# Performance work log

Hardware: AMD Instinct MI355X
Metric: run time of the kernel (lower is better)

The kernel has to match this reference:

```python
import jax, jax.numpy as jnp
import numpy as np

B, T, LEADS = 16, 3600, 12
P = 9; S = T // P          # 400 patches
DP = 128                   # d_patch / codebook dim
DM = 256                   # d_model
H = 8; HD = DM // H        # heads, head_dim
NL = 6                     # transformer layers
V = 512                    # codebook size
RH = 64                    # residual CNN hidden
BETA = 0.25


def conv1d(x, w, b, pad, stride=1):
    # x: (B,C,T), w: (O,I,K) pytorch layout
    y = jax.lax.conv_general_dilated(x, w, (stride,), [(pad, pad)],
                                     dimension_numbers=('NCH', 'OIH', 'NCH'))
    return y + b[None, :, None]


def layer_norm(x, g, b, eps=1e-5):
    m = jnp.mean(x, -1, keepdims=True)
    v = jnp.mean(jnp.square(x - m), -1, keepdims=True)
    return (x - m) * jax.lax.rsqrt(v + eps) * g + b


def gelu(x):
    return jax.nn.gelu(x, approximate=False)  # matches torch nn.GELU default


def setup_inputs() -> dict:
    key = jax.random.key(0)
    ks = iter(jax.random.split(key, 64))
    def rn(shape, s=0.02):
        return (s * jax.random.normal(next(ks), shape)).astype(jnp.float32)
    inp = {}
    inp['x'] = jax.random.normal(next(ks), (B, T, LEADS), dtype=jnp.float32)
    # PatchEncoder
    inp['pe_w1'] = rn((DP // 2, LEADS, 3)); inp['pe_b1'] = rn((DP // 2,))
    inp['pe_w2'] = rn((DP, DP // 2, 3));    inp['pe_b2'] = rn((DP,))
    inp['pe_pw'] = rn((DP, DP, P));         inp['pe_pb'] = rn((DP,))
    inp['pe_g'] = jnp.ones((DP,), jnp.float32); inp['pe_bb'] = jnp.zeros((DP,), jnp.float32)
    # VQ codebook (uniform +-1/V as in torch init)
    inp['cb'] = jax.random.uniform(next(ks), (V, DP), jnp.float32, -1.0 / V, 1.0 / V)
    # token_proj
    inp['tp_w'] = rn((DM, DP)); inp['tp_b'] = rn((DM,))
    inp['tp_g'] = jnp.ones((DM,), jnp.float32); inp['tp_bb'] = jnp.zeros((DM,), jnp.float32)
    # transformer layers (stacked over NL)
    inp['ln1_g'] = jnp.ones((NL, DM), jnp.float32); inp['ln1_b'] = jnp.zeros((NL, DM), jnp.float32)
    inp['inw'] = rn((NL, 3 * DM, DM));  inp['inb'] = rn((NL, 3 * DM))
    inp['ow'] = rn((NL, DM, DM));       inp['ob'] = rn((NL, DM))
    inp['ln2_g'] = jnp.ones((NL, DM), jnp.float32); inp['ln2_b'] = jnp.zeros((NL, DM), jnp.float32)
    inp['f1w'] = rn((NL, 4 * DM, DM));  inp['f1b'] = rn((NL, 4 * DM))
    inp['f2w'] = rn((NL, DM, 4 * DM));  inp['f2b'] = rn((NL, DM))
    inp['slopes'] = (1.0 + 0.1 * jax.random.normal(next(ks), (NL, H))).astype(jnp.float32)
    # final norm
    inp['fn_g'] = jnp.ones((DM,), jnp.float32); inp['fn_b'] = jnp.zeros((DM,), jnp.float32)
    # PatchDecoder: ConvTranspose1d weight (in=DM, out=DM//2, k=P)
    inp['up_w'] = rn((DM, DM // 2, P)); inp['up_b'] = rn((DM // 2,))
    inp['d1w'] = rn((DM // 4, DM // 2, 5)); inp['d1b'] = rn((DM // 4,))
    inp['d2w'] = rn((LEADS, DM // 4, 3));   inp['d2b'] = rn((LEADS,))
    # ResidualCNN
    inp['r1w'] = rn((RH, LEADS, 7)); inp['r1b'] = rn((RH,))
    inp['r2w'] = rn((RH, RH, 5));    inp['r2b'] = rn((RH,))
    inp['r3w'] = rn((RH, RH, 3));    inp['r3b'] = rn((RH,))
    inp['r4w'] = rn((LEADS, RH, 1)); inp['r4b'] = rn((LEADS,))
    inp['alpha'] = jnp.float32(0.5)
    return inp


def _forward(x, pe_w1, pe_b1, pe_w2, pe_b2, pe_pw, pe_pb, pe_g, pe_bb, cb,
             tp_w, tp_b, tp_g, tp_bb, ln1_g, ln1_b, inw, inb, ow, ob,
             ln2_g, ln2_b, f1w, f1b, f2w, f2b, slopes, fn_g, fn_b,
             up_w, up_b, d1w, d1b, d2w, d2b,
             r1w, r1b, r2w, r2b, r3w, r3b, r4w, r4b, alpha):
    Bs = x.shape[0]
    sg = jax.lax.stop_gradient
    # --- PatchEncoder: (B,T,L) -> (B,S,DP) ---
    h = x.transpose(0, 2, 1)                      # (B,L,T)
    h = gelu(conv1d(h, pe_w1, pe_b1, 1))
    h = gelu(conv1d(h, pe_w2, pe_b2, 1))
    h = conv1d(h, pe_pw, pe_pb, 0, stride=P)      # (B,DP,S)
    z_e = layer_norm(h.transpose(0, 2, 1), pe_g, pe_bb)   # (B,S,DP)
    # --- VQ codebook with STE ---
    zf = z_e.reshape(-1, DP)
    dist = (jnp.sum(zf * zf, 1, keepdims=True) + jnp.sum(cb * cb, 1)[None, :]
            - 2.0 * zf @ cb.T)                    # (B*S, V)
    tokens = jnp.argmin(dist, axis=1)
    zq = cb[tokens]                               # (B*S, DP)
    commit = jnp.mean(jnp.square(sg(zq) - zf)) + BETA * jnp.mean(jnp.square(zq - sg(zf)))
    zq_ste = (zf + sg(zq - zf)).reshape(Bs, S, DP)
    # --- token projection ---
    h = layer_norm(zq_ste @ tp_w.T + tp_b, tp_g, tp_bb)   # (B,S,DM)
    # --- transformer with relative-position bias ---
    pos = jnp.arange(S)
    rel = jnp.abs(pos[:, None] - pos[None, :]).astype(h.dtype)  # (S,S)
    scale = 1.0 / jnp.sqrt(jnp.float32(HD))
    for l in range(NL):
        bias = -jnp.abs(slopes[l])[:, None, None] * rel[None]   # (H,S,S)
        xn = layer_norm(h, ln1_g[l], ln1_b[l])
        qkv = xn @ inw[l].T + inb[l]
        q, k, v = jnp.split(qkv, 3, axis=-1)
        q = q.reshape(Bs, S, H, HD); k = k.reshape(Bs, S, H, HD); v = v.reshape(Bs, S, H, HD)
        logits = jnp.einsum('bqhd,bkhd->bhqk', q, k) * scale + bias[None]
        attn = jax.nn.softmax(logits, axis=-1)
        o = jnp.einsum('bhqk,bkhd->bqhd', attn, v).reshape(Bs, S, DM)
        h = h + o @ ow[l].T + ob[l]
        hn = layer_norm(h, ln2_g[l], ln2_b[l])
        h = h + gelu(hn @ f1w[l].T + f1b[l]) @ f2w[l].T + f2b[l]
    h = layer_norm(h, fn_g, fn_b)
    # --- PatchDecoder: (B,S,DM) -> (B,T,L) ---
    hc = h.transpose(0, 2, 1)                     # (B,DM,S)
    # ConvTranspose1d with stride==kernel==P, no overlap -> pure einsum
    u = jnp.einsum('bds,dok->bosk', hc, up_w).reshape(Bs, DM // 2, S * P) + up_b[None, :, None]
    u = gelu(u)
    u = gelu(conv1d(u, d1w, d1b, 2))
    u = conv1d(u, d2w, d2b, 1)                    # (B,L,T)
    decoded = u.transpose(0, 2, 1)
    # --- ResidualCNN on raw input ---
    r = x.transpose(0, 2, 1)
    r = gelu(conv1d(r, r1w, r1b, 3))
    r = gelu(conv1d(r, r2w, r2b, 2))
    r = gelu(conv1d(r, r3w, r3b, 1))
    r = conv1d(r, r4w, r4b, 0)
    residual = r.transpose(0, 2, 1)
    out = decoded + alpha * residual
    return out, commit


def reference(x, pe_w1, pe_b1, pe_w2, pe_b2, pe_pw, pe_pb, pe_g, pe_bb, cb,
              tp_w, tp_b, tp_g, tp_bb, ln1_g, ln1_b, inw, inb, ow, ob,
              ln2_g, ln2_b, f1w, f1b, f2w, f2b, slopes, fn_g, fn_b,
              up_w, up_b, d1w, d1b, d2w, d2b,
              r1w, r1b, r2w, r2b, r3w, r3b, r4w, r4b, alpha):
    return _forward(x, pe_w1, pe_b1, pe_w2, pe_b2, pe_pw, pe_pb, pe_g, pe_bb, cb,
                    tp_w, tp_b, tp_g, tp_bb, ln1_g, ln1_b, inw, inb, ow, ob,
                    ln2_g, ln2_b, f1w, f1b, f2w, f2b, slopes, fn_g, fn_b,
                    up_w, up_b, d1w, d1b, d2w, d2b,
                    r1w, r1b, r2w, r2b, r3w, r3b, r4w, r4b, alpha)
```

## Files before the change

kernel.cpp:

```cpp
#include <hip/hip_runtime.h>
#include <hip/hip_bf16.h>
#include <math.h>

#define BATCH 16
#define TLEN 3600
#define LEADS 12
#define PP 9
#define SS 400
#define DP 128
#define DM 256
#define NH 8
#define HD 32
#define NLAY 6
#define VV 512
#define RH 64

typedef __attribute__((ext_vector_type(8))) short short8b;
typedef __attribute__((ext_vector_type(4))) float f32x4;

__device__ __forceinline__ float gelu_f(float x) {
    return 0.5f * x * (1.0f + erff(x * 0.70710678118654752f));
}

__device__ __forceinline__ unsigned short f2bf(float f) {
// ... 151 lines not shown
                l8[e] = (short)f2bf(vv[e] - bf2f(h));
            }
        }
        *(short8b*)&Ah[row][q * 8] = h8;
        *(short8b*)&Al[row][q * 8] = l8;
    }
    f32x4 acc[2][8];
    #pragma unroll
    for (int i = 0; i < 2; ++i)
        #pragma unroll
        for (int j = 0; j < 8; ++j) acc[i][j] = (f32x4){0.f, 0.f, 0.f, 0.f};
    for (int k = 0; k < 3; ++k) {
        __syncthreads();
        for (int u = tid; u < 128 * 8; u += 256) {
            int co = u >> 3, q = u & 7;
            *(short8b*)&Wh_s[co][q * 8] = *(const short8b*)&wh[((size_t)(k * 128 + co)) * 64 + q * 8];
            *(short8b*)&Wl_s[co][q * 8] = *(const short8b*)&wl[((size_t)(k * 128 + co)) * 64 + q * 8];
        }
        __syncthreads();
        #pragma unroll
        for (int c32 = 0; c32 < 2; ++c32) {
            short8b ah0 = *(const short8b*)&Ah[w * 32 + fr + k][c32 * 32 + kg];
            short8b ah1 = *(const short8b*)&Ah[w * 32 + 16 + fr + k][c32 * 32 + kg];
            short8b al0 = *(const short8b*)&Al[w * 32 + fr + k][c32 * 32 + kg];
            short8b al1 = *(const short8b*)&Al[w * 32 + 16 + fr + k][c32 * 32 + kg];
            #pragma unroll
            for (int j = 0; j < 8; ++j) {
                short8b bh = *(const short8b*)&Wh_s[j * 16 + fr][c32 * 32 + kg];
                short8b bl = *(const short8b*)&Wl_s[j * 16 + fr][c32 * 32 + kg];
                acc[0][j] = __builtin_amdgcn_mfma_f32_16x16x32_bf16(ah0, bh, acc[0][j], 0, 0, 0);
                acc[0][j] = __builtin_amdgcn_mfma_f32_16x16x32_bf16(ah0, bl, acc[0][j], 0, 0, 0);
                acc[0][j] = __builtin_amdgcn_mfma_f32_16x16x32_bf16(al0, bh, acc[0][j], 0, 0, 0);
                acc[1][j] = __builtin_amdgcn_mfma_f32_16x16x32_bf16(ah1, bh, acc[1][j], 0, 0, 0);
                acc[1][j] = __builtin_amdgcn_mfma_f32_16x16x32_bf16(ah1, bl, acc[1][j], 0, 0, 0);
                acc[1][j] = __builtin_amdgcn_mfma_f32_16x16x32_bf16(al1, bh, acc[1][j], 0, 0, 0);
            }
        }
    }
    const int orow = (lane >> 4) * 4, ocol = lane & 15;
    #pragma unroll
    for (int i = 0; i < 2; ++i)
        #pragma unroll
        for (int j = 0; j < 8; ++j) {
            const int co = j * 16 + ocol;
            const float bv = bias[co];
            #pragma unroll
            for (int r = 0; r < 4; ++r) {
                int t = t0 + w * 32 + i * 16 + orow + r;
                if (t < TLEN) {
                    int s = t / PP, kk = t - s * PP;
                    out[((size_t)(b * SS + s)) * 1152 + kk * 128 + co] = gelu_f(acc[i][j][r] + bv);
                }
            }
        }
}

__global__ void pwpack3_k(const float* __restrict__ pw,
                          unsigned short* __restrict__ wh,
                          unsigned short* __restrict__ wl) {
    int idx = blockIdx.x * 256 + threadIdx.x;
    if (idx < 128 * 1152) {
        int n = idx % 1152, d = idx / 1152;
        int co = n & 127, kk = n >> 7;
        float v = pw[(size_t)d * 1152 + co * 9 + kk];
        unsigned short h = f2bf(v);
        wh[idx] = h;
        wl[idx] = f2bf(v - bf2f(h));
    }
}

__global__ __launch_bounds__(256) void pproj3_k(const float* __restrict__ A,
                                                const unsigned short* __restrict__ Wh,
                                                const unsigned short* __restrict__ Wl,
                                                float* __restrict__ Cp,
                                                int M) {
    __shared__ __align__(16) unsigned short Ah[128][40];
    __shared__ __align__(16) unsigned short Al[128][40];
    __shared__ __align__(16) unsigned short Bh[128][40];
    __shared__ __align__(16) unsigned short Bl[128][40];
    const int tid = threadIdx.x;
    const int gm0 = blockIdx.y * 128;
    const int z = blockIdx.z;
    const int w = tid >> 6, lane = tid & 63;
    const int wr0 = (w >> 1) * 64, wc0 = (w & 1) * 64;
    const int srow = tid >> 1, sc = (tid & 1) * 16;
    const int K = 1152;
    const int kb = z * 192;
    f32x4 acc[4][4];
    #pragma unroll
    for (int i = 0; i < 4; ++i)
        #pragma unroll
        for (int j = 0; j < 4; ++j) acc[i][j] = (f32x4){0.f, 0.f, 0.f, 0.f};
    const int fr = lane & 15, kg = (lane >> 4) * 8;
    for (int s = 0; s < 6; ++s) {
        const int k0 = kb + s * 32;
        __syncthreads();
        {
            const float* ga = A + (size_t)(gm0 + srow) * K + k0 + sc;
            #pragma unroll
            for (int g = 0; g < 2; ++g) {
                float4 v0 = *(const float4*)(ga + g * 8);
                float4 v1 = *(const float4*)(ga + g * 8 + 4);
                short8b h8, l8;
                float vv[8] = {v0.x, v0.y, v0.z, v0.w, v1.x, v1.y, v1.z, v1.w};
                #pragma unroll
                for (int e = 0; e < 8; ++e) {
                    unsigned short h = f2bf(vv[e]);
                    h8[e] = (short)h;
                    l8[e] = (short)f2bf(vv[e] - bf2f(h));
                }
                *(short8b*)&Ah[srow][sc + g * 8] = h8;
                *(short8b*)&Al[srow][sc + g * 8] = l8;
            }
            const unsigned short* gh = Wh + (size_t)srow * K + k0 + sc;
            const unsigned short* gl = Wl + (size_t)srow * K + k0 + sc;
            *(short8b*)&Bh[srow][sc] = *(const short8b*)gh;
            *(short8b*)&Bh[srow][sc + 8] = *(const short8b*)(gh + 8);
            *(short8b*)&Bl[srow][sc] = *(const short8b*)gl;
            *(short8b*)&Bl[srow][sc + 8] = *(const short8b*)(gl + 8);
        }
        __syncthreads();
        short8b afh[4], afl[4], bfh[4], bfl[4];
        #pragma unroll
        for (int i = 0; i < 4; ++i) {
            afh[i] = *(const short8b*)&Ah[wr0 + i * 16 + fr][kg];
            afl[i] = *(const short8b*)&Al[wr0 + i * 16 + fr][kg];
            bfh[i] = *(const short8b*)&Bh[wc0 + i * 16 + fr][kg];
            bfl[i] = *(const short8b*)&Bl[wc0 + i * 16 + fr][kg];
        }
        #pragma unroll
        for (int i = 0; i < 4; ++i)
            #pragma unroll
            for (int j = 0; j < 4; ++j) {
                acc[i][j] = __builtin_amdgcn_mfma_f32_16x16x32_bf16(afh[i], bfh[j], acc[i][j], 0, 0, 0);
                acc[i][j] = __builtin_amdgcn_mfma_f32_16x16x32_bf16(afh[i], bfl[j], acc[i][j], 0, 0, 0);
                acc[i][j] = __builtin_amdgcn_mfma_f32_16x16x32_bf16(afl[i], bfh[j], acc[i][j], 0, 0, 0);
            }
    }
    const int orow = (lane >> 4) * 4, ocol = lane & 15;
    float* Cz = Cp + (size_t)z * M * 128;
    #pragma unroll
    for (int i = 0; i < 4; ++i)
        #pragma unroll
        for (int j = 0; j < 4; ++j) {
            const int colg = wc0 + j * 16 + ocol;
            #pragma unroll
            for (int r = 0; r < 4; ++r) {
                const int rowg = gm0 + wr0 + i * 16 + orow + r;
                Cz[(size_t)rowg * 128 + colg] = acc[i][j][r];
            }
        }
}

template <int CI, int K, int PAD>
__global__ __launch_bounds__(256) void mfconv_k(const unsigned short* __restrict__ in,
                                                const unsigned short* __restrict__ wpk,
                                                const float* __restrict__ bias,
                                                unsigned short* __restrict__ out) {
    constexpr int CIC = (CI > 64) ? 64 : CI;
    constexpr int NCH = CI / CIC;
    constexpr int TROWS = 128 + K - 1;
    constexpr int CQ = CIC / 8;
    __shared__ __align__(16) unsigned short in_s[TROWS][CIC + 8];
    __shared__ __align__(16) unsigned short w_s[K][64][CIC + 8];
    const int b = blockIdx.z;
    const int t0 = blockIdx.x * 128;
    const int tid = threadIdx.x;
    const int w = tid >> 6, lane = tid & 63;
    const int fr = lane & 15, kg = (lane >> 4) * 8;
    f32x4 acc[2][4];
    #pragma unroll
    for (int i = 0; i < 2; ++i)
        #pragma unroll
        for (int j = 0; j < 4; ++j) acc[i][j] = (f32x4){0.f, 0.f, 0.f, 0.f};
    for (int ch = 0; ch < NCH; ++ch) {
        const int c0 = ch * CIC;
        if (ch) __syncthreads();
        for (int u = tid; u < TROWS * CQ; u += 256) {
            int row = u / CQ, q = u - row * CQ;
            int t = t0 + row - PAD;
            short8b v = (short8b){0, 0, 0, 0, 0, 0, 0, 0};
            if (t >= 0 && t < TLEN)
                v = *(const short8b*)&in[((size_t)(b * TLEN + t)) * CI + c0 + q * 8];
            *(short8b*)&in_s[row][q * 8] = v;
        }
        for (int u = tid; u < K * 64 * CQ; u += 256) {
            int q = u % CQ; int rest = u / CQ; int co = rest & 63; int k = rest >> 6;
            *(short8b*)&w_s[k][co][q * 8] =
                *(const short8b*)&wpk[((size_t)(k * 64 + co)) * CI + c0 + q * 8];
        }
        __syncthreads();
        #pragma unroll
        for (int k = 0; k < K; ++k) {
            #pragma unroll
            for (int c32 = 0; c32 < CIC / 32; ++c32) {
                short8b a0 = *(const short8b*)&in_s[w * 32 + fr + k][c32 * 32 + kg];
                short8b a1 = *(const short8b*)&in_s[w * 32 + 16 + fr + k][c32 * 32 + kg];
                short8b b0 = *(const short8b*)&w_s[k][fr][c32 * 32 + kg];
                short8b b1 = *(const short8b*)&w_s[k][16 + fr][c32 * 32 + kg];
                short8b b2 = *(const short8b*)&w_s[k][32 + fr][c32 * 32 + kg];
                short8b b3 = *(const short8b*)&w_s[k][48 + fr][c32 * 32 + kg];
                acc[0][0] = __builtin_amdgcn_mfma_f32_16x16x32_bf16(a0, b0, acc[0][0], 0, 0, 0);
                acc[0][1] = __builtin_amdgcn_mfma_f32_16x16x32_bf16(a0, b1, acc[0][1], 0, 0, 0);
                acc[0][2] = __builtin_amdgcn_mfma_f32_16x16x32_bf16(a0, b2, acc[0][2], 0, 0, 0);
                acc[0][3] = __builtin_amdgcn_mfma_f32_16x16x32_bf16(a0, b3, acc[0][3], 0, 0, 0);
                acc[1][0] = __builtin_amdgcn_mfma_f32_16x16x32_bf16(a1, b0, acc[1][0], 0, 0, 0);
                acc[1][1] = __builtin_amdgcn_mfma_f32_16x16x32_bf16(a1, b1, acc[1][1], 0, 0, 0);
                acc[1][2] = __builtin_amdgcn_mfma_f32_16x16x32_bf16(a1, b2, acc[1][2], 0, 0, 0);
                acc[1][3] = __builtin_amdgcn_mfma_f32_16x16x32_bf16(a1, b3, acc[1][3], 0, 0, 0);
            }
        }
    }
    const int orow = (lane >> 4) * 4, ocol = lane & 15;
    #pragma unroll
    for (int i = 0; i < 2; ++i)
        #pragma unroll
        for (int j = 0; j < 4; ++j) {
            const int co = j * 16 + ocol;
            const float bv = bias[co];
            #pragma unroll
            for (int r = 0; r < 4; ++r) {
                int t = t0 + w * 32 + i * 16 + orow + r;
                if (t < TLEN)
                    out[((size_t)(b * TLEN + t)) * 64 + co] = f2bf(gelu_f(acc[i][j][r] + bv));
            }
        }
}

template <int ACT, int RES, int OUTBF>
__global__ __launch_bounds__(256) void bgemm_k(const unsigned short* __restrict__ A,
                                               const unsigned short* __restrict__ W,
                                               const float* __restrict__ bias,
                                               const float* __restrict__ res,
                                               void* __restrict__ Cv,
                                               int M, int N, int K) {
    __shared__ __align__(16) unsigned short As[128][40];
    __shared__ __align__(16) unsigned short Bs[128][40];
    const int tid = threadIdx.x;
    const int gm0 = blockIdx.y * 128, gn0 = blockIdx.x * 128;
    const int w = tid >> 6, lane = tid & 63;
    const int wr0 = (w >> 1) * 64, wc0 = (w & 1) * 64;
    const int srow = tid >> 1, sc = (tid & 1) * 16;
    const unsigned short* ga = A + (size_t)(gm0 + srow) * K + sc;
    const unsigned short* gb = W + (size_t)(gn0 + srow) * K + sc;
    short8b ra0 = *(const short8b*)(ga), ra1 = *(const short8b*)(ga + 8);
    short8b rb0 = *(const short8b*)(gb), rb1 = *(const short8b*)(gb + 8);
    f32x4 acc[4][4];
    #pragma unroll
    for (int i = 0; i < 4; ++i)
        #pragma unroll
        for (int j = 0; j < 4; ++j) acc[i][j] = (f32x4){0.f, 0.f, 0.f, 0.f};
    const int fr = lane & 15, kg = (lane >> 4) * 8;
    const int nstep = K >> 5;
    for (int s = 0; s < nstep; ++s) {
        __syncthreads();
        *(short8b*)&As[srow][sc] = ra0; *(short8b*)&As[srow][sc + 8] = ra1;
        *(short8b*)&Bs[srow][sc] = rb0; *(short8b*)&Bs[srow][sc + 8] = rb1;
        __syncthreads();
        if (s + 1 < nstep) {
            ga += 32; gb += 32;
            ra0 = *(const short8b*)(ga); ra1 = *(const short8b*)(ga + 8);
            rb0 = *(const short8b*)(gb); rb1 = *(const short8b*)(gb + 8);
        }
        short8b af[4], bf[4];
        #pragma unroll
        for (int i = 0; i < 4; ++i) {
            af[i] = *(const short8b*)&As[wr0 + i * 16 + fr][kg];
            bf[i] = *(const short8b*)&Bs[wc0 + i * 16 + fr][kg];
        }
        #pragma unroll
        for (int i = 0; i < 4; ++i)
            #pragma unroll
            for (int j = 0; j < 4; ++j)
                acc[i][j] = __builtin_amdgcn_mfma_f32_16x16x32_bf16(af[i], bf[j], acc[i][j], 0, 0, 0);
    }
    const int orow = (lane >> 4) * 4, ocol = lane & 15;
    #pragma unroll
    for (int i = 0; i < 4; ++i) {
        #pragma unroll
        for (int j = 0; j < 4; ++j) {
            const int colg = gn0 + wc0 + j * 16 + ocol;
            const float bsv = bias[colg];
            #pragma unroll
            for (int r = 0; r < 4; ++r) {
                const int rowg = gm0 + wr0 + i * 16 + orow + r;
                float v = acc[i][j][r] + bsv;
                if (ACT) v = gelu_f(v);
                if (RES) v += res[(size_t)rowg * N + colg];
                if (OUTBF) ((unsigned short*)Cv)[(size_t)rowg * N + colg] = f2bf(v);
                else ((float*)Cv)[(size_t)rowg * N + colg] = v;
            }
        }
    }
}

__global__ void tobf_k(const float* __restrict__ in, unsigned short* __restrict__ out, int n) {
    int i = blockIdx.x * 256 + threadIdx.x;
    if (i < n) out[i] = f2bf(in[i]);
}

__global__ void cpack_k(const float* __restrict__ w, unsigned short* __restrict__ out,
                        int Co, int CI, int K) {
    int idx = blockIdx.x * 256 + threadIdx.x;
    if (idx < Co * CI * K) {
        int ci = idx % CI; int rest = idx / CI; int co = rest % Co; int k = rest / Co;
        out[idx] = f2bf(w[((size_t)co * CI + ci) * K + k]);
    }
}

__global__ void upwt2_k(const float* __restrict__ w, const float* __restrict__ bsrc,
                        unsigned short* __restrict__ out, float* __restrict__ b2) {
    int idx = blockIdx.x * 256 + threadIdx.x;
    if (idx < 1152 * 256) {
        int d = idx & 255, n = idx >> 8;
        int o = n & 127, k = n >> 7;
        out[(size_t)n * 256 + d] = f2bf(w[(size_t)d * 1152 + o * 9 + k]);
    }
    if (idx < 1152) b2[idx] = bsrc[idx & 127];
}

__global__ __launch_bounds__(128) void ln128s_k(const float* __restrict__ part,
                                                const float* __restrict__ bias,
                                                const float* __restrict__ g,
                                                const float* __restrict__ bb,
                                                float* __restrict__ out,
                                                int M) {
    int row = blockIdx.x, tid = threadIdx.x;
    __shared__ float sm[2];
    size_t stride = (size_t)M * DP;
    size_t base = (size_t)row * DP + tid;
    float v = bias[tid];
    #pragma unroll
    for (int s2 = 0; s2 < 6; ++s2) v += part[base + (size_t)s2 * stride];
    float mean = block_sum_128(v, sm) * (1.0f / DP);
    float d = v - mean;
    float var = block_sum_128(d * d, sm) * (1.0f / DP);
    out[(size_t)row * DP + tid] = d * rsqrtf(var + 1e-5f) * g[tid] + bb[tid];
}

__global__ void cbnorm_k(const float* __restrict__ cb, float* __restrict__ cbn) {
    int c = blockIdx.x * 256 + threadIdx.x;
    if (c < VV) {
        const float* cr = cb + (size_t)c * DP;
        float s = 0;
        for (int i = 0; i < DP; ++i) s += cr[i] * cr[i];
        cbn[c] = s;
    }
}

__global__ __launch_bounds__(256) void vq2_k(const float* __restrict__ ze,
                                             const float* __restrict__ cb,
                                             const float* __restrict__ cbn,
                                             unsigned short* __restrict__ zqb,
                                             float* __restrict__ vqs) {
    __shared__ __align__(16) float z_s[32][132];
    __shared__ __align__(16) float cb_s[64][132];
    __shared__ float cbn_s[64];
    __shared__ float bval[256];
    __shared__ int bidx[256];
    __shared__ int tok_s[32];
    __shared__ float psum[256];
    const int tid = threadIdx.x;
    const int r0 = blockIdx.x * 32;
    const int r = tid >> 3, cs = tid & 7;
    for (int idx = tid; idx < 32 * 128; idx += 256) {
        int rr = idx >> 7, cc = idx & 127;
        z_s[rr][cc] = ze[((size_t)(r0 + rr)) * DP + cc];
    }
    float best = 1e30f; int bi = 0;
    for (int c0 = 0; c0 < VV; c0 += 64) {
        __syncthreads();
        for (int idx = tid; idx < 64 * 128; idx += 256) {
            int rr = idx >> 7, cc = idx & 127;
            cb_s[rr][cc] = cb[((size_t)(c0 + rr)) * DP + cc];
        }
        if (tid < 64) cbn_s[tid] = cbn[c0 + tid];
        __syncthreads();
        float dot[8] = {};
        for (int i = 0; i < 128; i += 4) {
            float4 zv = *(const float4*)&z_s[r][i];
            #pragma unroll
            for (int j = 0; j < 8; ++j) {
                float4 cv = *(const float4*)&cb_s[cs + 8 * j][i];
                dot[j] += zv.x * cv.x + zv.y * cv.y + zv.z * cv.z + zv.w * cv.w;
            }
        }
        #pragma unroll
        for (int j = 0; j < 8; ++j) {
            float dist = cbn_s[cs + 8 * j] - 2.0f * dot[j];
            if (dist < best) { best = dist; bi = c0 + cs + 8 * j; }
        }
    }
    bval[tid] = best; bidx[tid] = bi;
    __syncthreads();
    if (cs == 0) {
        float bv = bval[tid]; int bix = bidx[tid];
        #pragma unroll
        for (int j = 1; j < 8; ++j) {
            float v = bval[tid + j]; int ix = bidx[tid + j];
            if (v < bv || (v == bv && ix < bix)) { bv = v; bix = ix; }
        }
        tok_s[r] = bix;
    }
    __syncthreads();
    int tok = tok_s[r];
    float part = 0;
    const float* cr = cb + (size_t)tok * DP + cs * 16;
    #pragma unroll
    for (int i = 0; i < 16; i += 4) {
        float4 qv = *(const float4*)(cr + i);
        float4 zv = *(const float4*)&z_s[r][cs * 16 + i];
        float dx = qv.x - zv.x, dy = qv.y - zv.y, dz = qv.z - zv.z, dw = qv.w - zv.w;
        part += dx * dx + dy * dy + dz * dz + dw * dw;
        size_t ob = ((size_t)(r0 + r)) * DP + cs * 16 + i;
        zqb[ob + 0] = f2bf(qv.x); zqb[ob + 1] = f2bf(qv.y);
        zqb[ob + 2] = f2bf(qv.z); zqb[ob + 3] = f2bf(qv.w);
    }
    psum[tid] = part;
    __syncthreads();
    if (cs == 0) {
        float s = 0;
        #pragma unroll
        for (int j = 0; j < 8; ++j) s += psum[tid + j];
        vqs[r0 + r] = s;
    }
}

__global__ void vqreduce_k(const float* __restrict__ vqs, float* __restrict__ out) {
    float s = 0;
    for (int i = threadIdx.x; i < BATCH * SS; i += 256) s += vqs[i];
    __shared__ float sm[4];
    s = block_sum_256(s, sm);
    if (threadIdx.x == 0) out[0] = s * (1.25f / (float)(BATCH * SS * DP));
}

template <int OUTBF>
__global__ __launch_bounds__(256) void lnw_k(const float* __restrict__ in,
                                             const float* __restrict__ g,
                                             const float* __restrict__ bb,
                                             void* __restrict__ out) {
    const int row = blockIdx.x * 4 + (threadIdx.x >> 6);
    const int lane = threadIdx.x & 63;
    float4 v = *(const float4*)&in[(size_t)row * DM + lane * 4];
    float s = v.x + v.y + v.z + v.w;
    #pragma unroll
    for (int o = 1; o < 64; o <<= 1) s += __shfl_xor(s, o);
    float mean = s * (1.0f / DM);
    float dx = v.x - mean, dy = v.y - mean, dz = v.z - mean, dw = v.w - mean;
    float vv = dx * dx + dy * dy + dz * dz + dw * dw;
    #pragma unroll
    for (int o = 1; o < 64; o <<= 1) vv += __shfl_xor(vv, o);
    float rstd = rsqrtf(vv * (1.0f / DM) + 1e-5f);
    float4 gv = *(const float4*)&g[lane * 4];
    float4 bv = *(const float4*)&bb[lane * 4];
    float o0 = dx * rstd * gv.x + bv.x;
    float o1 = dy * rstd * gv.y + bv.y;
    float o2 = dz * rstd * gv.z + bv.z;
    float o3 = dw * rstd * gv.w + bv.w;
    if (OUTBF) {
        unsigned long long pk = (unsigned long long)f2bf(o0)
                              | ((unsigned long long)f2bf(o1) << 16)
                              | ((unsigned long long)f2bf(o2) << 32)
                              | ((unsigned long long)f2bf(o3) << 48);
        *(unsigned long long*)((unsigned short*)out + (size_t)row * DM + lane * 4) = pk;
    } else {
        float4 o4; o4.x = o0; o4.y = o1; o4.z = o2; o4.w = o3;
        *(float4*)((float*)out + (size_t)row * DM + lane * 4) = o4;
    }
}

__global__ __launch_bounds__(256) void fattn2_k(const unsigned short* __restrict__ qkv,
                                                const float* __restrict__ slopes,
                                                unsigned short* __restrict__ out) {
    __shared__ __align__(16) unsigned short Qs[128][40];
    __shared__ __align__(16) unsigned short Ks[64][40];
    __shared__ __align__(16) unsigned short Vt[32][72];
    __shared__ __align__(16) unsigned short Ps[4][32][72];
    const int qb = blockIdx.x, hh = blockIdx.y, b = blockIdx.z;
    const int tid = threadIdx.x;
    const int w = tid >> 6, lane = tid & 63;
    const int lr = lane & 15, lg = lane >> 4;
    const float slope = fabsf(slopes[hh]);
    const unsigned short* base = qkv + (size_t)b * SS * (3 * DM);
    {
        int row = tid >> 1, c = (tid & 1) * 16;
        int q = qb * 128 + row; q = q < SS ? q : SS - 1;
        const unsigned short* src = base + (size_t)q * (3 * DM) + hh * HD + c;
        *(short8b*)&Qs[row][c] = *(const short8b*)src;
        *(short8b*)&Qs[row][c + 8] = *(const short8b*)(src + 8);
    }
    __syncthreads();
    short8b qa[2];
    qa[0] = *(const short8b*)&Qs[w * 32 + lr][lg * 8];
    qa[1] = *(const short8b*)&Qs[w * 32 + 16 + lr][lg * 8];
    float m_run[2][4], l_run[2][4];
    #pragma unroll
    for (int f = 0; f < 2; ++f)
        #pragma unroll
        for (int r = 0; r < 4; ++r) { m_run[f][r] = -1e30f; l_run[f][r] = 0.f; }
    f32x4 of0[2], of1[2];
    of0[0] = of0[1] = of1[0] = of1[1] = (f32x4){0.f, 0.f, 0.f, 0.f};
    const int qg0[2] = { qb * 128 + w * 32 + lg * 4, qb * 128 + w * 32 + 16 + lg * 4 };
    for (int kt = 0; kt < SS; kt += 64) {
        const int tl = (SS - kt) < 64 ? (SS - kt) : 64;
        const int nks = tl >> 4;
        __syncthreads();
        {
            int row = tid >> 2, c = (tid & 3) * 8;
            if (row < tl) {
                *(short8b*)&Ks[row][c] =
                    *(const short8b*)(base + (size_t)(kt + row) * (3 * DM) + DM + hh * HD + c);
                short8b v8 = *(const short8b*)(base + (size_t)(kt + row) * (3 * DM) + 2 * DM + hh * HD + c);
                #pragma unroll
                for (int j = 0; j < 8; ++j) Vt[c + j][row] = ((unsigned short*)&v8)[j];
            }
        }
        __syncthreads();
        f32x4 sf[2][4];
        #pragma unroll
        for (int ks = 0; ks < 4; ++ks) {
            if (ks < nks) {
                short8b kb8 = *(const short8b*)&Ks[ks * 16 + lr][lg * 8];
                sf[0][ks] = __builtin_amdgcn_mfma_f32_16x16x32_bf16(qa[0], kb8, (f32x4){0.f, 0.f, 0.f, 0.f}, 0, 0, 0);
                sf[1][ks] = __builtin_amdgcn_mfma_f32_16x16x32_bf16(qa[1], kb8, (f32x4){0.f, 0.f, 0.f, 0.f}, 0, 0, 0);
            }
        }
        #pragma unroll
        for (int f = 0; f < 2; ++f) {
            float pv[4][4];
            #pragma unroll
            for (int r = 0; r < 4; ++r) {
                float tmax = -1e30f;
                #pragma unroll
                for (int ks = 0; ks < 4; ++ks) {
                    if (ks < nks) {
                        float sv = sf[f][ks][r] * 0.17677669529663687f
                                 - slope * fabsf((float)(qg0[f] + r - (kt + ks * 16 + lr)));
                        pv[ks][r] = sv;
                        tmax = fmaxf(tmax, sv);
                    }
                }
                #pragma unroll
                for (int o = 1; o < 16; o <<= 1) tmax = fmaxf(tmax, __shfl_xor(tmax, o));
                float mnew = fmaxf(m_run[f][r], tmax);
                float sc = __expf(m_run[f][r] - mnew);
                m_run[f][r] = mnew;
                float tsum = 0.f;
                #pragma unroll
                for (int ks = 0; ks < 4; ++ks) {
                    if (ks < nks) {
                        float e = __expf(pv[ks][r] - mnew);
                        pv[ks][r] = e;
                        tsum += e;
                    }
                }
                #pragma unroll
                for (int o = 1; o < 16; o <<= 1) tsum += __shfl_xor(tsum, o);
                l_run[f][r] = l_run[f][r] * sc + tsum;
                of0[f][r] *= sc; of1[f][r] *= sc;
            }
            #pragma unroll
            for (int ks = 0; ks < 4; ++ks)
                #pragma unroll
                for (int r = 0; r < 4; ++r)
                    Ps[w][f * 16 + lg * 4 + r][ks * 16 + lr] = (ks < nks) ? f2bf(pv[ks][r]) : (unsigned short)0;
        }
        #pragma unroll
        for (int kc = 0; kc < 64; kc += 32) {
            if (kc < nks * 16) {
                short8b vb0 = *(const short8b*)&Vt[lr][kc + lg * 8];
                short8b vb1 = *(const short8b*)&Vt[16 + lr][kc + lg * 8];
                #pragma unroll
                for (int f = 0; f < 2; ++f) {
                    short8b pa = *(const short8b*)&Ps[w][f * 16 + lr][kc + lg * 8];
                    of0[f] = __builtin_amdgcn_mfma_f32_16x16x32_bf16(pa, vb0, of0[f], 0, 0, 0);
                    of1[f] = __builtin_amdgcn_mfma_f32_16x16x32_bf16(pa, vb1, of1[f], 0, 0, 0);
                }
            }
        }
    }
    #pragma unroll
    for (int f = 0; f < 2; ++f)
        #pragma unroll
        for (int r = 0; r < 4; ++r) {
            int q = qg0[f] + r;
            if (q < SS) {
                float inv = 1.0f / l_run[f][r];
                out[((size_t)(b * SS + q)) * DM + hh * HD + lr] = f2bf(of0[f][r] * inv);
                out[((size_t)(b * SS + q)) * DM + hh * HD + 16 + lr] = f2bf(of1[f][r] * inv);
            }
        }
}

__global__ __launch_bounds__(256) void final2_k(const unsigned short* __restrict__ ud1,
                                                const unsigned short* __restrict__ r3i,
                                                const float* __restrict__ d2w,
                                                const float* __restrict__ d2b,
                                                const float* __restrict__ r4w,
                                                const float* __restrict__ r4b,
                                                const float* __restrict__ alpha,
                                                float* __restrict__ out) {
    __shared__ float u_s[64][66];
    __shared__ float r_s[64][64];
    __shared__ float wd_s[64][3][12];
    __shared__ float wr_s[64][12];
    __shared__ float o_s[64][12];
    const int b = blockIdx.z, t0 = blockIdx.x * 64, tid = threadIdx.x;
    for (int u2 = tid; u2 < 66 * 8; u2 += 256) {
        int j = u2 >> 3, q = u2 & 7;
        int t = t0 + j - 1;
        short8b v = (short8b){0, 0, 0, 0, 0, 0, 0, 0};
        if (t >= 0 && t < TLEN) v = *(const short8b*)&ud1[((size_t)(b * TLEN + t)) * 64 + q * 8];
        #pragma unroll
        for (int i = 0; i < 8; ++i) u_s[q * 8 + i][j] = bf2f((unsigned short)v[i]);
    }
    for (int u2 = tid; u2 < 64 * 8; u2 += 256) {
        int j = u2 >> 3, q = u2 & 7;
        int t = t0 + j;
        short8b v = (short8b){0, 0, 0, 0, 0, 0, 0, 0};
        if (t < TLEN) v = *(const short8b*)&r3i[((size_t)(b * TLEN + t)) * 64 + q * 8];
        #pragma unroll
        for (int i = 0; i < 8; ++i) r_s[q * 8 + i][j] = bf2f((unsigned short)v[i]);
    }
    for (int idx = tid; idx < 64 * 3 * 12; idx += 256) {
        int l = idx % 12, k = (idx / 12) % 3, ci = idx / 36;
        wd_s[ci][k][l] = d2w[(l * 64 + ci) * 3 + k];
    }
    for (int idx = tid; idx < 64 * 12; idx += 256) {
        int l = idx % 12, ci = idx / 12;
        wr_s[ci][l] = r4w[l * 64 + ci];
    }
    __syncthreads();
    const int tl = tid & 63, lg = tid >> 6;
    float accD[3] = {}, accR[3] = {};
    for (int ci = 0; ci < 64; ++ci) {
        float a0 = u_s[ci][tl], a1 = u_s[ci][tl + 1], a2 = u_s[ci][tl + 2];
        float rv = r_s[ci][tl];
        #pragma unroll
        for (int c = 0; c < 3; ++c) {
            int l = lg * 3 + c;
            accD[c] += a0 * wd_s[ci][0][l] + a1 * wd_s[ci][1][l] + a2 * wd_s[ci][2][l];
            accR[c] = fmaf(rv, wr_s[ci][l], accR[c]);
        }
    }
    float al = alpha[0];
    #pragma unroll
    for (int c = 0; c < 3; ++c) {
        int l = lg * 3 + c;
        o_s[tl][l] = accD[c] + d2b[l] + al * (accR[c] + r4b[l]);
    }
    __syncthreads();
    for (int idx = tid; idx < 64 * 12; idx += 256) {
        int t = t0 + idx / 12;
        if (t < TLEN) out[((size_t)b * TLEN + t) * 12 + idx % 12] = o_s[idx / 12][idx % 12];
    }
}

extern "C" void kernel_launch(void* const* d_in, const int* in_sizes, int n_in,
                              void* d_out, int out_size, void* d_ws, size_t ws_size,
                              hipStream_t stream) {
    const float* x     = (const float*)d_in[0];
    const float* pe_w1 = (const float*)d_in[1];
    const float* pe_b1 = (const float*)d_in[2];
    const float* pe_w2 = (const float*)d_in[3];
    const float* pe_b2 = (const float*)d_in[4];
    const float* pe_pw = (const float*)d_in[5];
    const float* pe_pb = (const float*)d_in[6];
    const float* pe_g  = (const float*)d_in[7];
    const float* pe_bb = (const float*)d_in[8];
    const float* cb    = (const float*)d_in[9];
    const float* tp_w  = (const float*)d_in[10];
    const float* tp_b  = (const float*)d_in[11];
    const float* tp_g  = (const float*)d_in[12];
    const float* tp_bb = (const float*)d_in[13];
    const float* ln1_g = (const float*)d_in[14];
    const float* ln1_b = (const float*)d_in[15];
    const float* inw   = (const float*)d_in[16];
    const float* inb   = (const float*)d_in[17];
    const float* ow    = (const float*)d_in[18];
    const float* ob    = (const float*)d_in[19];
    const float* ln2_g = (const float*)d_in[20];
    const float* ln2_b = (const float*)d_in[21];
    const float* f1w   = (const float*)d_in[22];
    const float* f1b   = (const float*)d_in[23];
    const float* f2w   = (const float*)d_in[24];
    const float* f2b   = (const float*)d_in[25];
    const float* slopes= (const float*)d_in[26];
    const float* fn_g  = (const float*)d_in[27];
    const float* fn_b  = (const float*)d_in[28];
    const float* up_w  = (const float*)d_in[29];
    const float* up_b  = (const float*)d_in[30];
    const float* d1w   = (const float*)d_in[31];
    const float* d1b   = (const float*)d_in[32];
    const float* d2w   = (const float*)d_in[33];
    const float* d2b   = (const float*)d_in[34];
    const float* r1w   = (const float*)d_in[35];
    const float* r1b   = (const float*)d_in[36];
    const float* r2w   = (const float*)d_in[37];
    const float* r2b   = (const float*)d_in[38];
    const float* r3w   = (const float*)d_in[39];
    const float* r3b   = (const float*)d_in[40];
    const float* r4w   = (const float*)d_in[41];
    const float* r4b   = (const float*)d_in[42];
    const float* alpha = (const float*)d_in[43];

    float* W = (float*)d_ws;
    size_t off = 0;
    auto alloc = [&](size_t n) { float* p = W + off; off += (n + 3) & ~(size_t)3; return p; };
    const size_t M = (size_t)BATCH * SS;
    float* A    = alloc((size_t)BATCH * DP * TLEN);
    float* Bb   = alloc((size_t)BATCH * 64 * TLEN);
    float* ze   = alloc(M * DP);
    float* tx   = alloc(M * DM);
    float* hb   = alloc(M * DM);
    float* qf   = alloc(M * 3 * DM);
    float* cbn  = alloc(VV);
    float* vqs  = alloc(M);
    float* upb2 = alloc(1152);
    unsigned short* zqb  = (unsigned short*)alloc(M * DP / 2);
    unsigned short* xnb  = (unsigned short*)alloc(M * DM / 2);
    unsigned short* aob  = (unsigned short*)alloc(M * DM / 2);
    float* pgpart        = qf;
    unsigned short* qkvb = (unsigned short*)qf;
    unsigned short* ffb  = (unsigned short*)qf;
    unsigned short* utm  = (unsigned short*)qf;
    unsigned short* inwb = (unsigned short*)alloc((size_t)NLAY * 3 * DM * DM / 2);
    unsigned short* owb  = (unsigned short*)alloc((size_t)NLAY * DM * DM / 2);
    unsigned short* f1wb = (unsigned short*)alloc((size_t)NLAY * 4 * DM * DM / 2);
    unsigned short* f2wb = (unsigned short*)alloc((size_t)NLAY * 4 * DM * DM / 2);
    unsigned short* tpwb = (unsigned short*)alloc((size_t)DM * DP / 2);
    unsigned short* upwb = (unsigned short*)alloc((size_t)1152 * DM / 2);
    unsigned short* pwh  = (unsigned short*)alloc((size_t)128 * 1152 / 2);
    unsigned short* pwl  = (unsigned short*)alloc((size_t)128 * 1152 / 2);
    unsigned short* w2h  = (unsigned short*)alloc((size_t)3 * 128 * 64 / 2);
    unsigned short* w2l  = (unsigned short*)alloc((size_t)3 * 128 * 64 / 2);
    unsigned short* r2pk = (unsigned short*)alloc((size_t)64 * 64 * 5 / 2);
    unsigned short* r3pk = (unsigned short*)alloc((size_t)64 * 64 * 3 / 2 + 2);
    unsigned short* d1pk = (unsigned short*)alloc((size_t)64 * 128 * 5 / 2);
    unsigned short* r1tm = (unsigned short*)alloc((size_t)BATCH * TLEN * 64 / 2);
    unsigned short* r2tm = (unsigned short*)alloc((size_t)BATCH * TLEN * 64 / 2);
    unsigned short* r3tm = (unsigned short*)alloc((size_t)BATCH * TLEN * 64 / 2);
    unsigned short* d1tm = (unsigned short*)alloc((size_t)BATCH * TLEN * 64 / 2);
    if (off * sizeof(float) > ws_size) return;

    float* outp = (float*)d_out;
    const dim3 cgrid(57, 1, BATCH);
    const dim3 mgrid(29, 1, BATCH);

    tobf_k<<<(NLAY * 3 * DM * DM + 255) / 256, 256, 0, stream>>>(inw, inwb, NLAY * 3 * DM * DM);
    tobf_k<<<(NLAY * DM * DM + 255) / 256, 256, 0, stream>>>(ow, owb, NLAY * DM * DM);
    tobf_k<<<(NLAY * 4 * DM * DM + 255) / 256, 256, 0, stream>>>(f1w, f1wb, NLAY * 4 * DM * DM);
    tobf_k<<<(NLAY * 4 * DM * DM + 255) / 256, 256, 0, stream>>>(f2w, f2wb, NLAY * 4 * DM * DM);
    tobf_k<<<(DM * DP + 255) / 256, 256, 0, stream>>>(tp_w, tpwb, DM * DP);
    upwt2_k<<<(1152 * 256 + 255) / 256, 256, 0, stream>>>(up_w, up_b, upwb, upb2);
    pwpack3_k<<<(128 * 1152 + 255) / 256, 256, 0, stream>>>(pe_pw, pwh, pwl);
    pwpack2_k<<<(3 * 128 * 64 + 255) / 256, 256, 0, stream>>>(pe_w2, w2h, w2l);
    cpack_k<<<(64 * 64 * 5 + 255) / 256, 256, 0, stream>>>(r2w, r2pk, 64, 64, 5);
    cpack_k<<<(64 * 64 * 3 + 255) / 256, 256, 0, stream>>>(r3w, r3pk, 64, 64, 3);
    cpack_k<<<(64 * 128 * 5 + 255) / 256, 256, 0, stream>>>(d1w, d1pk, 64, 128, 5);

    enc1_k<<<dim3(57, BATCH), 256, 0, stream>>>(x, pe_w1, pe_b1, r1w, r1b, Bb, r1tm);

    pe2m_k<<<dim3(29, BATCH), 256, 0, stream>>>(Bb, w2h, w2l, pe_b2, A);
    cbnorm_k<<<2, 256, 0, stream>>>(cb, cbn);
    pproj3_k<<<dim3(1, M / 128, 6), 256, 0, stream>>>(A, pwh, pwl, pgpart, M);
    ln128s_k<<<M, 128, 0, stream>>>(pgpart, pe_pb, pe_g, pe_bb, ze, M);
    vq2_k<<<M / 32, 256, 0, stream>>>(ze, cb, cbn, zqb, vqs);
    vqreduce_k<<<1, 256, 0, stream>>>(vqs, outp + (size_t)BATCH * TLEN * LEADS);

    mfconv_k<64, 5, 2><<<mgrid, 256, 0, stream>>>(r1tm, r2pk, r2b, r2tm);
    mfconv_k<64, 3, 1><<<mgrid, 256, 0, stream>>>(r2tm, r3pk, r3b, r3tm);

    bgemm_k<0, 0, 0><<<dim3(DM / 128, M / 128), 256, 0, stream>>>(zqb, tpwb, tp_b, nullptr, tx, M, DM, DP);
    lnw_k<0><<<M / 4, 256, 0, stream>>>(tx, tp_g, tp_bb, hb);

    for (int l = 0; l < NLAY; ++l) {
        lnw_k<1><<<M / 4, 256, 0, stream>>>(hb, ln1_g + l * DM, ln1_b + l * DM, xnb);
        bgemm_k<0, 0, 1><<<dim3(3 * DM / 128, M / 128), 256, 0, stream>>>(
            xnb, inwb + (size_t)l * 3 * DM * DM, inb + l * 3 * DM, nullptr, qkvb, M, 3 * DM, DM);
        fattn2_k<<<dim3((SS + 127) / 128, NH, BATCH), 256, 0, stream>>>(qkvb, slopes + l * NH, aob);
        bgemm_k<0, 1, 0><<<dim3(DM / 128, M / 128), 256, 0, stream>>>(
            aob, owb + (size_t)l * DM * DM, ob + l * DM, hb, hb, M, DM, DM);
        lnw_k<1><<<M / 4, 256, 0, stream>>>(hb, ln2_g + l * DM, ln2_b + l * DM, xnb);
        bgemm_k<1, 0, 1><<<dim3(4 * DM / 128, M / 128), 256, 0, stream>>>(
            xnb, f1wb + (size_t)l * 4 * DM * DM, f1b + l * 4 * DM, nullptr, ffb, M, 4 * DM, DM);
        bgemm_k<0, 1, 0><<<dim3(DM / 128, M / 128), 256, 0, stream>>>(
            ffb, f2wb + (size_t)l * 4 * DM * DM, f2b + l * DM, hb, hb, M, DM, 4 * DM);
    }
    lnw_k<1><<<M / 4, 256, 0, stream>>>(hb, fn_g, fn_b, xnb);

    bgemm_k<1, 0, 1><<<dim3(1152 / 128, M / 128), 256, 0, stream>>>(xnb, upwb, upb2, nullptr, utm, M, 1152, DM);
    mfconv_k<128, 5, 2><<<mgrid, 256, 0, stream>>>(utm, d1pk, d1b, d1tm);

    final2_k<<<cgrid, 256, 0, stream>>>(d1tm, r3tm, d2w, d2b, r4w, r4b, alpha, outp);
}
```

Before: 856.9 us.

## Move VQ nearest-codebook search onto MFMA with split-bf16 precision

Replaces the scalar FP32 VQ distance kernel with an MFMA-based GEMM. It splits the activations and codebook into bf16 hi/lo pairs and uses three MFMAs to keep near-FP32 accuracy. Each block handles 128 rows against 128 codes and writes a per-block argmin partial, and a new finalize kernel merges the partials, gathers the chosen codes and computes the commitment sum. The codebook hi/lo split is packed once up front. This adds two launches and partial buffers, and the split-bf16 dot products could flip argmin ties or near-ties compared with pure FP32.

```diff
diff --git a/kernel.cpp b/kernel.cpp
--- a/kernel.cpp
+++ b/kernel.cpp
@@ -327,6 +327,148 @@
         }
 }
 
+__global__ void cbpack_k(const float* __restrict__ cb,
+                         unsigned short* __restrict__ ch,
+                         unsigned short* __restrict__ cl) {
+    int idx = blockIdx.x * 256 + threadIdx.x;
+    if (idx < VV * DP) {
+        float v = cb[idx];
+        unsigned short h = f2bf(v);
+        ch[idx] = h;
+        cl[idx] = f2bf(v - bf2f(h));
+    }
+}
+
+__global__ __launch_bounds__(256) void vq3_k(const float* __restrict__ ze,
+                                             const unsigned short* __restrict__ ch,
+                                             const unsigned short* __restrict__ cl,
+                                             const float* __restrict__ cbn,
+                                             float* __restrict__ pval,
+                                             int* __restrict__ pidx,
+                                             int M) {
+    __shared__ __align__(16) unsigned short Ah[128][40];
+    __shared__ __align__(16) unsigned short Al[128][40];
+    __shared__ __align__(16) unsigned short Bh[128][40];
+    __shared__ __align__(16) unsigned short Bl[128][40];
+    __shared__ float bwv[128][2];
+    __shared__ int bwi[128][2];
+    const int tid = threadIdx.x;
+    const int c0 = blockIdx.x * 128;
+    const int gm0 = blockIdx.y * 128;
+    const int w = tid >> 6, lane = tid & 63;
+    const int wr0 = (w >> 1) * 64, wc0 = (w & 1) * 64;
+    const int srow = tid >> 1, sc = (tid & 1) * 16;
+    const int fr = lane & 15, kg = (lane >> 4) * 8;
+    f32x4 acc[4][4];
+    #pragma unroll
+    for (int i = 0; i < 4; ++i)
+        #pragma unroll
+        for (int j = 0; j < 4; ++j) acc[i][j] = (f32x4){0.f, 0.f, 0.f, 0.f};
+    for (int s = 0; s < 4; ++s) {
+        const int k0 = s * 32;
+        __syncthreads();
+        {
+            const float* ga = ze + (size_t)(gm0 + srow) * DP + k0 + sc;
+            #pragma unroll
+            for (int g = 0; g < 2; ++g) {
+                float4 v0 = *(const float4*)(ga + g * 8);
+                float4 v1 = *(const float4*)(ga + g * 8 + 4);
+                short8b h8, l8;
+                float vv[8] = {v0.x, v0.y, v0.z, v0.w, v1.x, v1.y, v1.z, v1.w};
+                #pragma unroll
+                for (int e = 0; e < 8; ++e) {
+                    unsigned short h = f2bf(vv[e]);
+                    h8[e] = (short)h;
+                    l8[e] = (short)f2bf(vv[e] - bf2f(h));
+                }
+                *(short8b*)&Ah[srow][sc + g * 8] = h8;
+                *(short8b*)&Al[srow][sc + g * 8] = l8;
+            }
+            const unsigned short* gh = ch + (size_t)(c0 + srow) * DP + k0 + sc;
+            const unsigned short* gl = cl + (size_t)(c0 + srow) * DP + k0 + sc;
+            *(short8b*)&Bh[srow][sc] = *(const short8b*)gh;
+            *(short8b*)&Bh[srow][sc + 8] = *(const short8b*)(gh + 8);
+            *(short8b*)&Bl[srow][sc] = *(const short8b*)gl;
+            *(short8b*)&Bl[srow][sc + 8] = *(const short8b*)(gl + 8);
+        }
+        __syncthreads();
+        short8b afh[4], afl[4], bfh[4], bfl[4];
+        #pragma unroll
+        for (int i = 0; i < 4; ++i) {
+            afh[i] = *(const short8b*)&Ah[wr0 + i * 16 + fr][kg];
+            afl[i] = *(const short8b*)&Al[wr0 + i * 16 + fr][kg];
+            bfh[i] = *(const short8b*)&Bh[wc0 + i * 16 + fr][kg];
+            bfl[i] = *(const short8b*)&Bl[wc0 + i * 16 + fr][kg];
+        }
+        #pragma unroll
+        for (int i = 0; i < 4; ++i)
+            #pragma unroll
+            for (int j = 0; j < 4; ++j) {
+                acc[i][j] = __builtin_amdgcn_mfma_f32_16x16x32_bf16(afh[i], bfh[j], acc[i][j], 0, 0, 0);
+                acc[i][j] = __builtin_amdgcn_mfma_f32_16x16x32_bf16(afh[i], bfl[j], acc[i][j], 0, 0, 0);
+                acc[i][j] = __builtin_amdgcn_mfma_f32_16x16x32_bf16(afl[i], bfh[j], acc[i][j], 0, 0, 0);
+            }
+    }
+    const int orow = (lane >> 4) * 4, ocol = lane & 15;
+    #pragma unroll
+    for (int i = 0; i < 4; ++i)
+        #pragma unroll
+        for (int r = 0; r < 4; ++r) {
+            int row = wr0 + i * 16 + orow + r;
+            float bv = 1e30f; int bi = 0;
+            #pragma unroll
+            for (int j = 0; j < 4; ++j) {
+                int col = c0 + wc0 + j * 16 + ocol;
+                float d = cbn[col] - 2.0f * acc[i][j][r];
+                if (d < bv || (d == bv && col < bi)) { bv = d; bi = col; }
+            }
+            #pragma unroll
+            for (int o = 1; o < 16; o <<= 1) {
+                float ov = __shfl_xor(bv, o);
+                int oi = __shfl_xor(bi, o);
+                if (ov < bv || (ov == bv && oi < bi)) { bv = ov; bi = oi; }
+            }
+            if (ocol == 0) { bwv[row][w & 1] = bv; bwi[row][w & 1] = bi; }
+        }
+    __syncthreads();
+    if (tid < 128) {
+        float v0 = bwv[tid][0], v1 = bwv[tid][1];
+        int i0 = bwi[tid][0], i1 = bwi[tid][1];
+        bool sel = (v1 < v0) || (v1 == v0 && i1 < i0);
+        pval[(size_t)blockIdx.x * M + gm0 + tid] = sel ? v1 : v0;
+        pidx[(size_t)blockIdx.x * M + gm0 + tid] = sel ? i1 : i0;
+    }
+}
+
+__global__ __launch_bounds__(128) void vqfin_k(const float* __restrict__ ze,
+                                               const float* __restrict__ cb,
+                                               const float* __restrict__ pval,
+                                               const int* __restrict__ pidx,
+                                               unsigned short* __restrict__ zqb,
+                                               float* __restrict__ vqs,
+                                               int M) {
+    const int row = blockIdx.x, tid = threadIdx.x;
+    __shared__ float sm[2];
+    __shared__ int tok_s;
+    if (tid == 0) {
+        float bv = pval[row]; int bi = pidx[row];
+        #pragma unroll
+        for (int z = 1; z < 4; ++z) {
+            float v = pval[(size_t)z * M + row]; int ix = pidx[(size_t)z * M + row];
+            if (v < bv || (v == bv && ix < bi)) { bv = v; bi = ix; }
+        }
+        tok_s = bi;
+    }
+    __syncthreads();
+    int tok = tok_s;
+    float qv = cb[(size_t)tok * DP + tid];
+    float zv = ze[(size_t)row * DP + tid];
+    zqb[(size_t)row * DP + tid] = f2bf(qv);
+    float d = qv - zv;
+    float tot = block_sum_128(d * d, sm);
+    if (tid == 0) vqs[row] = tot;
+}
+
 template <int CI, int K, int PAD>
 __global__ __launch_bounds__(256) void mfconv_k(const unsigned short* __restrict__ in,
                                                 const unsigned short* __restrict__ wpk,
@@ -520,84 +662,6 @@
         float s = 0;
         for (int i = 0; i < DP; ++i) s += cr[i] * cr[i];
         cbn[c] = s;
-    }
-}
-
-__global__ __launch_bounds__(256) void vq2_k(const float* __restrict__ ze,
-                                             const float* __restrict__ cb,
-                                             const float* __restrict__ cbn,
-                                             unsigned short* __restrict__ zqb,
-                                             float* __restrict__ vqs) {
-    __shared__ __align__(16) float z_s[32][132];
-    __shared__ __align__(16) float cb_s[64][132];
-    __shared__ float cbn_s[64];
-    __shared__ float bval[256];
-    __shared__ int bidx[256];
-    __shared__ int tok_s[32];
-    __shared__ float psum[256];
-    const int tid = threadIdx.x;
-    const int r0 = blockIdx.x * 32;
-    const int r = tid >> 3, cs = tid & 7;
-    for (int idx = tid; idx < 32 * 128; idx += 256) {
-        int rr = idx >> 7, cc = idx & 127;
-        z_s[rr][cc] = ze[((size_t)(r0 + rr)) * DP + cc];
-    }
-    float best = 1e30f; int bi = 0;
-    for (int c0 = 0; c0 < VV; c0 += 64) {
-        __syncthreads();
-        for (int idx = tid; idx < 64 * 128; idx += 256) {
-            int rr = idx >> 7, cc = idx & 127;
-            cb_s[rr][cc] = cb[((size_t)(c0 + rr)) * DP + cc];
-        }
-        if (tid < 64) cbn_s[tid] = cbn[c0 + tid];
-        __syncthreads();
-        float dot[8] = {};
-        for (int i = 0; i < 128; i += 4) {
-            float4 zv = *(const float4*)&z_s[r][i];
-            #pragma unroll
-            for (int j = 0; j < 8; ++j) {
-                float4 cv = *(const float4*)&cb_s[cs + 8 * j][i];
-                dot[j] += zv.x * cv.x + zv.y * cv.y + zv.z * cv.z + zv.w * cv.w;
-            }
-        }
-        #pragma unroll
-        for (int j = 0; j < 8; ++j) {
-            float dist = cbn_s[cs + 8 * j] - 2.0f * dot[j];
-            if (dist < best) { best = dist; bi = c0 + cs + 8 * j; }
-        }
-    }
-    bval[tid] = best; bidx[tid] = bi;
-    __syncthreads();
-    if (cs == 0) {
-        float bv = bval[tid]; int bix = bidx[tid];
-        #pragma unroll
-        for (int j = 1; j < 8; ++j) {
-            float v = bval[tid + j]; int ix = bidx[tid + j];
-            if (v < bv || (v == bv && ix < bix)) { bv = v; bix = ix; }
-        }
-        tok_s[r] = bix;
-    }
-    __syncthreads();
-    int tok = tok_s[r];
-    float part = 0;
-    const float* cr = cb + (size_t)tok * DP + cs * 16;
-    #pragma unroll
-    for (int i = 0; i < 16; i += 4) {
-        float4 qv = *(const float4*)(cr + i);
-        float4 zv = *(const float4*)&z_s[r][cs * 16 + i];
-        float dx = qv.x - zv.x, dy = qv.y - zv.y, dz = qv.z - zv.z, dw = qv.w - zv.w;
-        part += dx * dx + dy * dy + dz * dz + dw * dw;
-        size_t ob = ((size_t)(r0 + r)) * DP + cs * 16 + i;
-        zqb[ob + 0] = f2bf(qv.x); zqb[ob + 1] = f2bf(qv.y);
-        zqb[ob + 2] = f2bf(qv.z); zqb[ob + 3] = f2bf(qv.w);
-    }
-    psum[tid] = part;
-    __syncthreads();
-    if (cs == 0) {
-        float s = 0;
-        #pragma unroll
-        for (int j = 0; j < 8; ++j) s += psum[tid + j];
-        vqs[r0 + r] = s;
     }
 }
 
@@ -892,6 +956,8 @@
     float* cbn  = alloc(VV);
     float* vqs  = alloc(M);
     float* upb2 = alloc(1152);
+    float* pval = alloc(4 * M);
+    int*   pidx = (int*)alloc(4 * M);
     unsigned short* zqb  = (unsigned short*)alloc(M * DP / 2);
     unsigned short* xnb  = (unsigned short*)alloc(M * DM / 2);
     unsigned short* aob  = (unsigned short*)alloc(M * DM / 2);
@@ -909,6 +975,8 @@
     unsigned short* pwl  = (unsigned short*)alloc((size_t)128 * 1152 / 2);
     unsigned short* w2h  = (unsigned short*)alloc((size_t)3 * 128 * 64 / 2);
     unsigned short* w2l  = (unsigned short*)alloc((size_t)3 * 128 * 64 / 2);
+    unsigned short* cbh  = (unsigned short*)alloc((size_t)VV * DP / 2);
+    unsigned short* cbl  = (unsigned short*)alloc((size_t)VV * DP / 2);
     unsigned short* r2pk = (unsigned short*)alloc((size_t)64 * 64 * 5 / 2);
     unsigned short* r3pk = (unsigned short*)alloc((size_t)64 * 64 * 3 / 2 + 2);
     unsigned short* d1pk = (unsigned short*)alloc((size_t)64 * 128 * 5 / 2);
@@ -930,6 +998,7 @@
     upwt2_k<<<(1152 * 256 + 255) / 256, 256, 0, stream>>>(up_w, up_b, upwb, upb2);
     pwpack3_k<<<(128 * 1152 + 255) / 256, 256, 0, stream>>>(pe_pw, pwh, pwl);
     pwpack2_k<<<(3 * 128 * 64 + 255) / 256, 256, 0, stream>>>(pe_w2, w2h, w2l);
+    cbpack_k<<<(VV * DP + 255) / 256, 256, 0, stream>>>(cb, cbh, cbl);
     cpack_k<<<(64 * 64 * 5 + 255) / 256, 256, 0, stream>>>(r2w, r2pk, 64, 64, 5);
     cpack_k<<<(64 * 64 * 3 + 255) / 256, 256, 0, stream>>>(r3w, r3pk, 64, 64, 3);
     cpack_k<<<(64 * 128 * 5 + 255) / 256, 256, 0, stream>>>(d1w, d1pk, 64, 128, 5);
@@ -940,7 +1009,8 @@
     cbnorm_k<<<2, 256, 0, stream>>>(cb, cbn);
     pproj3_k<<<dim3(1, M / 128, 6), 256, 0, stream>>>(A, pwh, pwl, pgpart, M);
     ln128s_k<<<M, 128, 0, stream>>>(pgpart, pe_pb, pe_g, pe_bb, ze, M);
-    vq2_k<<<M / 32, 256, 0, stream>>>(ze, cb, cbn, zqb, vqs);
+    vq3_k<<<dim3(4, M / 128), 256, 0, stream>>>(ze, cbh, cbl, cbn, pval, pidx, M);
+    vqfin_k<<<M, 128, 0, stream>>>(ze, cb, pval, pidx, zqb, vqs, M);
     vqreduce_k<<<1, 256, 0, stream>>>(vqs, outp + (size_t)BATCH * TLEN * LEADS);
 
     mfconv_k<64, 5, 2><<<mgrid, 256, 0, stream>>>(r1tm, r2pk, r2b, r2tm);
```

Result: faster. 825.3 us (-3.7%).
